# Kernel optimization log

Measured on AMD Instinct MI355X. Metric: run time of the kernel, lower is better.

Reference implementation:

```python
import jax, jax.numpy as jnp
import numpy as np

C = 768
HEADS = 12
NF = 8      # num_frames
SL = 196    # seq_len (patches per frame)
B = 2
N = 1 + NF * SL
HID = 4 * C


def _ln(x, g, b, eps=1e-5):
    mu = jnp.mean(x, axis=-1, keepdims=True)
    var = jnp.mean((x - mu) ** 2, axis=-1, keepdims=True)
    return (x - mu) * jax.lax.rsqrt(var + eps) * g + b


def setup_inputs() -> dict:
    key = jax.random.key(0)
    ks = jax.random.split(key, 16)
    s = 0.02
    return {
        "x": jax.random.normal(ks[0], (B, N, C), jnp.float32),
        "g1": jnp.ones((C,), jnp.float32),
        "b1": jnp.zeros((C,), jnp.float32),
        "Wqkv": jax.random.normal(ks[1], (C, 3 * C), jnp.float32) * s,
        "Wq": jax.random.normal(ks[2], (C, C), jnp.float32) * s,
        "Wkv": jax.random.normal(ks[3], (C, 2 * C), jnp.float32) * s,
        "Wp": jax.random.normal(ks[4], (C, C), jnp.float32) * s,
        "bp": jnp.zeros((C,), jnp.float32),
        "g2": jnp.ones((C,), jnp.float32),
        "b2": jnp.zeros((C,), jnp.float32),
        "W1": jax.random.normal(ks[5], (C, HID), jnp.float32) * s,
        "bf1": jnp.zeros((HID,), jnp.float32),
        "W2": jax.random.normal(ks[6], (HID, C), jnp.float32) * s,
        "bf2": jnp.zeros((C,), jnp.float32),
        "seq_len": SL,
        "num_frames": NF,
    }


def _traj_attn(xn, Wqkv, Wq, Wkv, Wp, bp, P, F):
    Bb, Nn, Cc = xn.shape
    h = HEADS
    d = Cc // h
    scale = d ** -0.5
    S = F * P  # non-cls tokens

    qkv = xn @ Wqkv                                   # (B,N,3C)
    q, k, v = jnp.split(qkv, 3, axis=-1)

    def heads(t):  # (B,N,C) -> (B*h, N, d)
        return t.reshape(Bb, Nn, h, d).transpose(0, 2, 1, 3).reshape(Bb * h, Nn, d)

    q, k, v = heads(q), heads(k), heads(v)
    cls_q, q_ = q[:, :1], q[:, 1:]
    k_ = k[:, 1:]
    v_ = v[:, 1:]

    # cls token attends to all tokens
    sim = jnp.einsum('bid,bjd->bij', cls_q * scale, k)
    cls_out = jnp.einsum('bij,bjd->bid', jax.nn.softmax(sim, axis=-1), v)
    cls_out = cls_out.reshape(Bb, h, 1, d).transpose(0, 2, 1, 3).reshape(Bb, 1, Cc)

    # stage 1: space-only softmax per frame
    qk = jnp.einsum('bqd,bkd->bqk', q_, k_).reshape(Bb * h, S, F, P)
    space_attn = jax.nn.softmax(scale * qk, axis=-1)          # (Bh,S,F,P)
    v_r = v_.reshape(Bb * h, F, P, d)
    x1 = jnp.einsum('bqfn,bfnd->bqfd', space_attn, v_r)       # (Bh,S,F,d)
    x1 = x1.reshape(Bb, h, S, F, d).transpose(0, 2, 3, 1, 4).reshape(Bb, S, F, Cc)

    # diagonal across (query-frame, key-frame)
    xg = x1.reshape(Bb, F, P, F, Cc)
    diag = jnp.diagonal(xg, axis1=1, axis2=3)                 # (B,P,C,F)
    x_diag = diag.transpose(0, 3, 1, 2).reshape(Bb, S, Cc)    # b (f n) d

    # stage 2: frame-wise attention
    q2 = (x_diag @ Wq).reshape(Bb, S, h, d).transpose(0, 2, 1, 3) * scale  # bhsd
    kv2 = x1 @ Wkv
    k2, v2 = jnp.split(kv2, 2, axis=-1)
    k2 = k2.reshape(Bb, S, F, h, d).transpose(0, 3, 1, 2, 4)  # bhsfd
    attn2 = jax.nn.softmax(jnp.einsum('bhsd,bhsfd->bhsf', q2, k2), axis=-1)
    xo = x1.reshape(Bb, S, F, h, d).transpose(0, 3, 1, 2, 4)  # use_original_code=True
    out = jnp.einsum('bhsf,bhsfd->bhsd', attn2, xo)
    out = out.transpose(0, 2, 1, 3).reshape(Bb, S, Cc)

    out = jnp.concatenate([cls_out, out], axis=1) @ Wp + bp
    return out


def reference(x, g1, b1, Wqkv, Wq, Wkv, Wp, bp, g2, b2, W1, bf1, W2, bf2, seq_len, num_frames):
    x = x + _traj_attn(_ln(x, g1, b1), Wqkv, Wq, Wkv, Wp, bp, seq_len, num_frames)
    h = _ln(x, g2, b2)
    h = jax.nn.gelu(h @ W1 + bf1, approximate=False) @ W2 + bf2
    return x + h
```

## Files before the change

### kernel.cpp

```cpp
#include <hip/hip_runtime.h>
#include <hip/hip_bf16.h>
#include <math.h>

#define C     768
#define HEADS 12
#define HD    64
#define NF    8
#define SL    196
#define BB    2
#define NN    1569
#define SS    1568
#define HID   3072
#define CLS_CH 256
#define CLS_NC 7
#define QSCALE 0.18033688011112042f

typedef __attribute__((ext_vector_type(8))) short short8;
typedef __attribute__((ext_vector_type(4))) float f32x4;
typedef unsigned short u16;
typedef unsigned int u32;

__device__ inline float fast_exp2(float x) { return __builtin_amdgcn_exp2f(x); }

__device__ inline u16 f2b(float f) {
    __hip_bfloat16 h = __float2bfloat16(f);
    return *reinterpret_cast<u16*>(&h);
}
__device__ inline float b2f(u16 u) {
    union { unsigned u; float f; } v; v.u = ((unsigned)u) << 16;
    return v.f;
}

__device__ inline void gload_lds16(const void* g, void* l) {
    __builtin_amdgcn_global_load_lds(
        (const __attribute__((address_space(1))) void*)g,
        (__attribute__((address_space(3))) void*)l, 16, 0, 0);
}

__global__ void ln_kernel(const float* __restrict__ x, const float* __restrict__ g,
                          const float* __restrict__ b, u16* __restrict__ out, int rows) {
    int row = blockIdx.x;
    if (row >= rows) return;
    const float* xr = x + (size_t)row * C;
    int tid = threadIdx.x;
    float v[3];
    float sum = 0.f, sumsq = 0.f;
#pragma unroll
    for (int i = 0; i < 3; i++) {
        v[i] = xr[tid + 256 * i];
        sum += v[i]; sumsq += v[i] * v[i];
    }
    __shared__ float s1[4], s2[4];
    for (int off = 32; off; off >>= 1) {
        sum   += __shfl_xor(sum, off);
        sumsq += __shfl_xor(sumsq, off);
    }
    int wave = tid >> 6, lane = tid & 63;
    if (lane == 0) { s1[wave] = sum; s2[wave] = sumsq; }
    __syncthreads();
    sum   = s1[0] + s1[1] + s1[2] + s1[3];
    sumsq = s2[0] + s2[1] + s2[2] + s2[3];
    float mu  = sum / C;
    float var = sumsq / C - mu * mu;
    float rstd = rsqrtf(fmaxf(var, 0.f) + 1e-5f);
    u16* outr = out + (size_t)row * C;
#pragma unroll
    for (int i = 0; i < 3; i++) {
        int c = tid + 256 * i;
        outr[c] = f2b((v[i] - mu) * rstd * g[c] + b[c]);
    }
}

__global__ void wtrans_all_kernel(
    const float* __restrict__ Wqkv, const float* __restrict__ Wq,
    const float* __restrict__ Wkv,  const float* __restrict__ Wp,
    const float* __restrict__ W1,   const float* __restrict__ W2,
    u16* Tqkv, u16* Tq, u16* Tkv, u16* Tp, u16* T1, u16* T2) {
    __shared__ float tile[64][65];
    int bid = blockIdx.x;
    const float* W; u16* Wt; int K, ldb, gx;
    if (bid < 432)       { W = Wqkv; Wt = Tqkv; K = 768;  ldb = 2304; gx = 36; }
    else if (bid < 576)  { W = Wq;   Wt = Tq;   K = 768;  ldb = 768;  gx = 12; bid -= 432; }
    else if (bid < 720)  { W = Wkv;  Wt = Tkv;  K = 768;  ldb = 1536; gx = 12; bid -= 576; }
    else if (bid < 864)  { W = Wp;   Wt = Tp;   K = 768;  ldb = 768;  gx = 12; bid -= 720; }
    else if (bid < 1440) { W = W1;   Wt = T1;   K = 768;  ldb = 3072; gx = 48; bid -= 864; }
    else                 { W = W2;   Wt = T2;   K = 3072; ldb = 768;  gx = 12; bid -= 1440; }
    int nb = (bid % gx) * 64, kb = (bid / gx) * 64;
    int tx = threadIdx.x & 63, ty = threadIdx.x >> 6;
#pragma unroll
    for (int i = 0; i < 64; i += 4)
        tile[ty + i][tx] = W[(size_t)(kb + ty + i) * ldb + nb + tx];
    __syncthreads();
#pragma unroll
    for (int i = 0; i < 64; i += 4)
        Wt[(size_t)(nb + ty + i) * K + kb + tx] = f2b(tile[tx][ty + i]);
}

template<int MODE, int BM, int BN>
__global__ __launch_bounds__(256) void gemm_bf16(
    const u16* __restrict__ A, const u16* __restrict__ Bt,
    const float* __restrict__ bias, const float* resid, void* Cout,
    int M, int N, int K, int lda, int ldb, int gx) {
    constexpr int MT   = BM / 32;
    constexpr int NT   = BN / 32;
    constexpr int ACH  = BM * 4;
    constexpr int TCH  = (BM + BN) * 4;
    constexpr int HALF = (BM + BN) * 64;
    __shared__ char smem[2 * HALF];
    int tid = threadIdx.x, lane = tid & 63, wave = tid >> 6;
    int wr = wave >> 1, wc = wave & 1;
    int r16 = lane & 15, kg = lane >> 4;

    int nwg = gridDim.x, orig = blockIdx.x;
    int qq = nwg >> 3, rr = nwg & 7, xcd = orig & 7, lid = orig >> 3;
    int wg = (xcd < rr ? xcd * (qq + 1) : rr * (qq + 1) + (xcd - rr) * qq) + lid;
    int bx = wg % gx, by = wg / gx;
    if constexpr (MODE == 4) {
        int mt_ = (M + BM - 1) / BM;
        int chunk = by / mt_; by -= chunk * mt_;
        A    += (size_t)chunk * K;
        Bt   += (size_t)chunk * K;
        Cout  = (void*)((float*)Cout + (size_t)chunk * ((size_t)M * N));
    }
    int row0 = by * BM, col0 = bx * BN;

    f32x4 acc[MT][NT];
#pragma unroll
    for (int mt = 0; mt < MT; mt++)
#pragma unroll
        for (int nt = 0; nt < NT; nt++) acc[mt][nt] = (f32x4){0.f, 0.f, 0.f, 0.f};

    auto stage = [&](char* dstbase, int ks) {
        int k0 = ks << 5;
#pragma unroll
        for (int it = 0; it < TCH / 256; it++) {
            int c = it * 256 + tid;
            const u16* src;
            if (c < ACH) {
                int ml = c >> 2, s = c & 3;
                int kgs = s ^ ((ml >> 1) & 3);
                int gm = row0 + ml; if (gm >= M) gm = M - 1;
                src = A + (size_t)gm * lda + k0 + kgs * 8;
            } else {
                int cc = c - ACH;
                int nl = cc >> 2, s = cc & 3;
                int kgs = s ^ ((nl >> 1) & 3);
                src = Bt + (size_t)(col0 + nl) * ldb + k0 + kgs * 8;
            }
            gload_lds16(src, dstbase + it * 4096 + wave * 1024);
        }
    };

    int nsteps = K >> 5;
    stage(smem, 0);
    __syncthreads();
    for (int ks = 0; ks < nsteps; ks++) {
        char* curb = smem + (ks & 1) * HALF;
        if (ks + 1 < nsteps) stage(smem + ((ks + 1) & 1) * HALF, ks + 1);
        short8 af[MT], bfr[NT];
#pragma unroll
        for (int mt = 0; mt < MT; mt++) {
            int ml = wr * (BM / 2) + mt * 16 + r16;
            af[mt] = *(const short8*)(curb + ml * 64 + ((kg ^ ((ml >> 1) & 3)) << 4));
        }
#pragma unroll
        for (int nt = 0; nt < NT; nt++) {
            int nl = wc * (BN / 2) + nt * 16 + r16;
            bfr[nt] = *(const short8*)(curb + BM * 64 + nl * 64 + ((kg ^ ((nl >> 1) & 3)) << 4));
        }
        __builtin_amdgcn_s_setprio(1);
#pragma unroll
        for (int mt = 0; mt < MT; mt++)
#pragma unroll
            for (int nt = 0; nt < NT; nt++)
                acc[mt][nt] = __builtin_amdgcn_mfma_f32_16x16x32_bf16(af[mt], bfr[nt], acc[mt][nt], 0, 0, 0);
        __builtin_amdgcn_s_setprio(0);
        __syncthreads();
    }
#pragma unroll
    for (int mt = 0; mt < MT; mt++) {
#pragma unroll
        for (int r2 = 0; r2 < 4; r2++) {
            int gm = row0 + wr * (BM / 2) + mt * 16 + kg * 4 + r2;
            if (gm >= M) continue;
#pragma unroll
            for (int nt = 0; nt < NT; nt++) {
                int gn = col0 + wc * (BN / 2) + nt * 16 + r16;
                float v = acc[mt][nt][r2];
                if constexpr (MODE == 1) {
                    v += bias[gn];
                    v = 0.5f * v * (1.f + erff(v * 0.70710678118f));
                }
                if constexpr (MODE == 2) {
                    v += bias[gn] + resid[(size_t)gm * N + gn];
                    ((float*)Cout)[(size_t)gm * N + gn] = v;
                } else if constexpr (MODE == 4) {
                    ((float*)Cout)[(size_t)gm * N + gn] = v;
                } else {
                    if constexpr (MODE == 3) { if (gn < 768) v *= QSCALE; }
                    ((u16*)Cout)[(size_t)gm * N + gn] = f2b(v);
                }
            }
        }
    }
}

__global__ void fc2_merge_kernel(const float* __restrict__ p,
                                 const float* __restrict__ bias, float* __restrict__ out) {
    int i = blockIdx.x * 256 + threadIdx.x;
    int total = BB * NN * (C / 4);
    if (i >= total) return;
    int c4 = i % (C / 4);
    size_t stride = (size_t)BB * NN * (C / 4);
    float4 bb = ((const float4*)bias)[c4];
    float4 a0 = ((const float4*)p)[i];
    float4 a1 = ((const float4*)p)[i + stride];
    float4 o  = ((float4*)out)[i];
    o.x += a0.x + a1.x + bb.x;
    o.y += a0.y + a1.y + bb.y;
    o.z += a0.z + a1.z + bb.z;
    o.w += a0.w + a1.w + bb.w;
    ((float4*)out)[i] = o;
}

__global__ void cls_partial_kernel(const u16* __restrict__ qkv, float* __restrict__ part) {
    int c = blockIdx.x, bh = blockIdx.y;
    int b = bh / HEADS, hh = bh % HEADS;
    int tid = threadIdx.x;
    int wave = tid >> 6, lane = tid & 63;
    __shared__ float s_q[HD];
    __shared__ float s_sc[CLS_CH];
    __shared__ float sm[4], ss[4];
    __shared__ float sacc[4][HD];
    if (tid < HD) s_q[tid] = b2f(qkv[(size_t)(b * NN) * 2304 + hh * HD + tid]);
    __syncthreads();

    int j0 = c * CLS_CH;
    int j = j0 + tid;
    float sc = -1e30f;
    if (j < NN) {
        const short8* kp = (const short8*)(qkv + ((size_t)(b * NN) + j) * 2304 + C + hh * HD);
        float acc = 0.f;
#pragma unroll
        for (int u = 0; u < 8; u++) {
            short8 kv = kp[u];
#pragma unroll
            for (int e = 0; e < 8; e++) acc += s_q[u * 8 + e] * b2f((u16)kv[e]);
        }
        sc = acc;
    }
    float m = sc;
    for (int off = 32; off; off >>= 1) m = fmaxf(m, __shfl_xor(m, off));
    if (lane == 0) sm[wave] = m;
    __syncthreads();
    m = fmaxf(fmaxf(sm[0], sm[1]), fmaxf(sm[2], sm[3]));
    float e = (j < NN) ? fast_exp2(sc - m) : 0.f;
    s_sc[tid] = e;
    float su = e;
    for (int off = 32; off; off >>= 1) su += __shfl_xor(su, off);
    if (lane == 0) ss[wave] = su;
    __syncthreads();
    float ssum = ss[0] + ss[1] + ss[2] + ss[3];

    int jj = tid >> 6, d = tid & 63;
    int jmax = NN - j0; if (jmax > CLS_CH) jmax = CLS_CH;
    const u16* vcol = qkv + ((size_t)(b * NN) + j0) * 2304 + 2 * C + hh * HD + d;
    float acc = 0.f;
    for (int t = jj; t < jmax; t += 4)
        acc += s_sc[t] * b2f(vcol[(size_t)t * 2304]);
    sacc[jj][d] = acc;
    __syncthreads();
    if (tid < HD) {
        float pv = sacc[0][tid] + sacc[1][tid] + sacc[2][tid] + sacc[3][tid];
        float* pp = part + ((size_t)bh * CLS_NC + c) * 66;
        pp[2 + tid] = pv;
        if (tid == 0) { pp[0] = m; pp[1] = ssum; }
    }
}

__global__ void cls_reduce_kernel(const float* __restrict__ part, u16* __restrict__ y) {
    int bh = blockIdx.x;
    int b = bh / HEADS, hh = bh % HEADS;
    int d = threadIdx.x;
    float gm = -1e30f;
#pragma unroll
    for (int c = 0; c < CLS_NC; c++)
        gm = fmaxf(gm, part[((size_t)bh * CLS_NC + c) * 66]);
    float tot = 0.f, pv = 0.f;
#pragma unroll
    for (int c = 0; c < CLS_NC; c++) {
        const float* pp = part + ((size_t)bh * CLS_NC + c) * 66;
        float w = fast_exp2(pp[0] - gm);
        tot += pp[1] * w;
        pv  += pp[2 + d] * w;
    }
    y[(size_t)(b * NN) * C + hh * HD + d] = f2b(pv / tot);
}

__global__ void repack_kv_kernel(const u16* __restrict__ qkv,
                                 u16* __restrict__ Kb, u16* __restrict__ Vt) {
    const int NK = 24 * NF * 208 * 8;
    const int NV = 24 * NF * 64 * 28;
    int t = blockIdx.x * 256 + threadIdx.x;
    if (t < NK) {
        int d8 = t & 7;
        int rest = t >> 3;
        int n = rest % 208;
        rest /= 208;
        int f = rest % NF;
        int bh = rest / NF;
        int b = bh / HEADS, h = bh % HEADS;
        short8 v = {0, 0, 0, 0, 0, 0, 0, 0};
        if (n < SL)
            v = *(const short8*)(qkv + ((size_t)(b * NN) + 1 + f * SL + n) * 2304 + C + h * HD + d8 * 8);
        *(short8*)(Kb + (((size_t)bh * NF + f) * 208 + n) * 64 + d8 * 8) = v;
    } else {
        int u = t - NK;
        if (u >= NV) return;
        int n8 = u % 28;
        int rest = u / 28;
        int d = rest % 64;
        rest /= 64;
        int f = rest % NF;
        int bh = rest / NF;
        int b = bh / HEADS, h = bh % HEADS;
        int n0 = n8 * 8;
        const u16* src = qkv + ((size_t)(b * NN) + 1 + f * SL) * 2304 + 2 * C + h * HD + d;
        short8 v;
#pragma unroll
        for (int jj = 0; jj < 8; jj++) {
            int n = n0 + jj;
            v[jj] = (n < SL) ? (short)src[(size_t)n * 2304] : (short)0;
        }
        *(short8*)(Vt + (((size_t)bh * NF + f) * 64 + d) * 224 + n0) = v;
    }
}

__global__ void space_attn_mfma(
    const u16* __restrict__ qkv, const u16* __restrict__ Kb,
    const u16* __restrict__ Vt, u16* __restrict__ x1, u16* __restrict__ xd) {
    __shared__ u16 smem[14848];
    int tid = threadIdx.x;
    int lane = tid & 63, wave = tid >> 6;
    int r16 = lane & 15, kg = lane >> 4;

    int n = blockIdx.x;
    int xcd = n & 7;
    int slot = n >> 3;
    int j = slot % 25;
    int gw = slot / 25;
    int bh = xcd * 3 + gw % 3;
    int f = gw / 3;
    int b = bh / HEADS, h = bh % HEADS;

    int strip = j * 4 + wave;
    bool act = strip < 98;
    if (!act) strip = 97;
    int q0 = strip * 16;

    const u16* qrow = qkv + ((size_t)(b * NN) + 1 + q0 + r16) * 2304 + h * HD + kg * 8;
    short8 aq0 = *(const short8*)(qrow);
    short8 aq1 = *(const short8*)(qrow + 32);

    const char* kb_g = (const char*)(Kb + ((size_t)bh * NF + f) * 208 * 64);
    for (int w = wave; w < 26; w += 4) {
        int p = w * 1024 + lane * 16;
        int row = p >> 7;
        int src = (p & ~127) | ((p & 127) ^ ((row & 7) << 4));
        gload_lds16(kb_g + src, (char*)smem + p);
    }
    __syncthreads();

    f32x4 acc[13];
#pragma unroll
    for (int t = 0; t < 13; t++) acc[t] = (f32x4){0.f, 0.f, 0.f, 0.f};
    const char* ksm = (const char*)smem;
    int swz = (r16 & 7) << 4;
    __builtin_amdgcn_s_setprio(1);
#pragma unroll
    for (int t = 0; t < 13; t++) {
        const char* krow = ksm + (t * 16 + r16) * 128;
        short8 bk0 = *(const short8*)(krow + ((kg * 16) ^ swz));
        short8 bk1 = *(const short8*)(krow + ((64 + kg * 16) ^ swz));
        acc[t] = __builtin_amdgcn_mfma_f32_16x16x32_bf16(bk0, aq0, acc[t], 0, 0, 0);
        acc[t] = __builtin_amdgcn_mfma_f32_16x16x32_bf16(bk1, aq1, acc[t], 0, 0, 0);
    }
    __builtin_amdgcn_s_setprio(0);

    const u16* vbase = Vt + ((size_t)bh * NF + f) * 64 * 224;
    short8 vf[2][4];
#pragma unroll
    for (int dt = 0; dt < 4; dt++)
        vf[0][dt] = *(const short8*)(vbase + (dt * 16 + r16) * 224 + kg * 8);

    __syncthreads();
    u16* pb = smem + wave * 3712;

    bool tailz = (kg >= 1);
    float ssum = 0.f;
    float pv_[13][4];
#pragma unroll
    for (int t = 0; t < 13; t++) {
#pragma unroll
        for (int r = 0; r < 4; r++) {
            float p = (t == 12 && tailz) ? 0.f : fast_exp2(acc[t][r]);
            pv_[t][r] = p;
            ssum += p;
        }
    }
    ssum += __shfl_xor(ssum, 16);
    ssum += __shfl_xor(ssum, 32);
    float inv = 1.f / ssum;

#pragma unroll
    for (int t = 0; t < 13; t++) {
        u32 w0 = (u32)f2b(pv_[t][0] * inv) | ((u32)f2b(pv_[t][1] * inv) << 16);
        u32 w1 = (u32)f2b(pv_[t][2] * inv) | ((u32)f2b(pv_[t][3] * inv) << 16);
        *(uint2*)(&pb[r16 * 232 + t * 16 + kg * 4]) = (uint2){w0, w1};
    }
    {
        int zr = lane >> 2, zc = 208 + (lane & 3) * 4;
        *(uint2*)(&pb[zr * 232 + zc]) = (uint2){0u, 0u};
    }

    f32x4 o[4];
#pragma unroll
    for (int dt = 0; dt < 4; dt++) o[dt] = (f32x4){0.f, 0.f, 0.f, 0.f};
    __builtin_amdgcn_s_setprio(1);
#pragma unroll
    for (int kc = 0; kc < 7; kc++) {
        if (kc < 6) {
#pragma unroll
            for (int dt = 0; dt < 4; dt++)
                vf[(kc + 1) & 1][dt] = *(const short8*)(vbase + (dt * 16 + r16) * 224 + (kc + 1) * 32 + kg * 8);
        }
        short8 pa = *(const short8*)(&pb[r16 * 232 + kc * 32 + kg * 8]);
#pragma unroll
        for (int dt = 0; dt < 4; dt++)
            o[dt] = __builtin_amdgcn_mfma_f32_16x16x32_bf16(pa, vf[kc & 1][dt], o[dt], 0, 0, 0);
    }
    __builtin_amdgcn_s_setprio(0);

    if (act) {
#pragma unroll
        for (int dt = 0; dt < 4; dt++)
#pragma unroll
            for (int r = 0; r < 4; r++)
                pb[(kg * 4 + r) * 72 + dt * 16 + r16] = f2b(o[dt][r]);
        u16* x1row = x1 + (((size_t)(b * SS + q0)) * NF + f) * C + h * HD;
        u16* xdrow = xd + ((size_t)(b * SS + q0)) * C + h * HD;
        int fbase = f * SL;
#pragma unroll
        for (int it = 0; it < 2; it++) {
            int c = it * 64 + lane;
            int qr = c >> 3, c8 = c & 7;
            short8 v8 = *(const short8*)(&pb[qr * 72 + c8 * 8]);
            *(short8*)(x1row + (size_t)qr * (NF * C) + c8 * 8) = v8;
            if ((unsigned)(q0 + qr - fbase) < (unsigned)SL)
                *(short8*)(xdrow + (size_t)qr * C + c8 * 8) = v8;
        }
    }
}

__global__ void attn2_kernel(const u16* __restrict__ q2, const u16* __restrict__ k2,
                             const u16* __restrict__ x1, u16* __restrict__ y) {
    int item = blockIdx.x * 4 + (threadIdx.x >> 6);
    if (item >= BB * HEADS * SS) return;
    int lane = threadIdx.x & 63;
    int s = item % SS;
    int bh = item / SS;
    int b = bh / HEADS, hh = bh % HEADS;
    size_t rowbs = (size_t)(b * SS + s);
    float qv = b2f(q2[rowbs * C + hh * HD + lane]) * QSCALE;
    float lg[NF];
#pragma unroll
    for (int f = 0; f < NF; f++) {
        float p = qv * b2f(k2[(rowbs * NF + f) * C + hh * HD + lane]);
        for (int off = 32; off; off >>= 1) p += __shfl_xor(p, off);
        lg[f] = p;
    }
    float m = lg[0];
#pragma unroll
    for (int f = 1; f < NF; f++) m = fmaxf(m, lg[f]);
    float sum = 0.f;
#pragma unroll
    for (int f = 0; f < NF; f++) { lg[f] = fast_exp2(lg[f] - m); sum += lg[f]; }
    float inv = 1.f / sum;
    float acc = 0.f;
#pragma unroll
    for (int f = 0; f < NF; f++) acc += lg[f] * b2f(x1[(rowbs * NF + f) * C + hh * HD + lane]);
    y[((size_t)(b * NN) + 1 + s) * C + hh * HD + lane] = f2b(acc * inv);
}

extern "C" void kernel_launch(void* const* d_in, const int* in_sizes, int n_in,
                              void* d_out, int out_size, void* d_ws, size_t ws_size,
                              hipStream_t stream) {
    const float* x    = (const float*)d_in[0];
    const float* g1   = (const float*)d_in[1];
    const float* b1   = (const float*)d_in[2];
    const float* Wqkv = (const float*)d_in[3];
    const float* Wq   = (const float*)d_in[4];
    const float* Wkv  = (const float*)d_in[5];
    const float* Wp   = (const float*)d_in[6];
    const float* bp   = (const float*)d_in[7];
    const float* g2   = (const float*)d_in[8];
    const float* b2_  = (const float*)d_in[9];
    const float* W1   = (const float*)d_in[10];
    const float* bf1  = (const float*)d_in[11];
    const float* W2   = (const float*)d_in[12];
    const float* bf2  = (const float*)d_in[13];
    float* out = (float*)d_out;

    u16* us     = (u16*)d_ws;
    u16* xn_b   = us;
    u16* qkv_b  = xn_b   + 2409984;
    u16* Wt_qkv = qkv_b  + 7229952;
    u16* Wt_q   = Wt_qkv + 1769472;
    u16* Wt_kv  = Wt_q   + 589824;
    u16* Wt_p   = Wt_kv  + 589824;
    u16* W1t    = Wt_p   + 589824;
    u16* W2t    = W1t    + 2359296;
    u16* Kb     = W2t    + 2359296;
    u16* Vt     = Kb     + 2555904;
    u16* x1b    = Vt     + 2752512;
    u16* xdb    = x1b    + 19267584;
    u16* q2b    = xdb    + 2408448;
    u16* k2b    = q2b    + 2408448;
    u16* y_b    = k2b    + 19267584;
    u16* a1b    = y_b    + 2409984;
    float* cls_ws   = (float*)(a1b + 9639936);
    float* fc2_part = cls_ws + 24 * 7 * 66;

    const int M1 = BB * NN;
    const int M2 = BB * SS;
    const int M3 = BB * SS * NF;

    wtrans_all_kernel<<<2016, 256, 0, stream>>>(Wqkv, Wq, Wkv, Wp, W1, W2,
                                                Wt_qkv, Wt_q, Wt_kv, Wt_p, W1t, W2t);
    ln_kernel<<<M1, 256, 0, stream>>>(x, g1, b1, xn_b, M1);
    gemm_bf16<3, 128, 64><<<36 * 25, 256, 0, stream>>>(
        xn_b, Wt_qkv, nullptr, nullptr, qkv_b, M1, 2304, 768, 768, 768, 36);
    repack_kv_kernel<<<(24 * NF * 208 * 8 + 24 * NF * 64 * 28 + 255) / 256, 256, 0, stream>>>(
        qkv_b, Kb, Vt);
    cls_partial_kernel<<<dim3(CLS_NC, BB * HEADS), 256, 0, stream>>>(qkv_b, cls_ws);
    cls_reduce_kernel<<<BB * HEADS, 64, 0, stream>>>(cls_ws, y_b);
    space_attn_mfma<<<4800, 256, 0, stream>>>(qkv_b, Kb, Vt, x1b, xdb);
    gemm_bf16<0, 64, 64><<<12 * 49, 256, 0, stream>>>(
        xdb, Wt_q, nullptr, nullptr, q2b, M2, 768, 768, 768, 768, 12);
    gemm_bf16<0, 128, 128><<<6 * 196, 256, 0, stream>>>(
        x1b, Wt_kv, nullptr, nullptr, k2b, M3, 768, 768, 768, 768, 6);
    attn2_kernel<<<(BB * HEADS * SS + 3) / 4, 256, 0, stream>>>(q2b, k2b, x1b, y_b);
    gemm_bf16<2, 64, 64><<<12 * 50, 256, 0, stream>>>(
        y_b, Wt_p, bp, x, out, M1, 768, 768, 768, 768, 12);
    ln_kernel<<<M1, 256, 0, stream>>>(out, g2, b2_, xn_b, M1);
    gemm_bf16<1, 128, 64><<<48 * 25, 256, 0, stream>>>(
        xn_b, W1t, bf1, nullptr, a1b, M1, 3072, 768, 768, 768, 48);
    gemm_bf16<4, 128, 64><<<12 * 25 * 2, 256, 0, stream>>>(
        a1b, W2t, nullptr, nullptr, fc2_part, M1, 768, 1536, 3072, 3072, 12);
    fc2_merge_kernel<<<(BB * NN * (C / 4) + 255) / 256, 256, 0, stream>>>(
        fc2_part, bf2, out);
}
```

Baseline: 291.8 us.

## Reassociate stage-2 logits to avoid the full K2 projection over all frames

Instead of projecting every x1 token through Wkv to build k2 (a large GEMM with M = B*S*F), the per-head query is folded into the key weights: u = q2_h · Wk_h^T is computed per head with a small GEMM. The logits are then taken as dot products of u with raw x1 rows inside a new fused attention kernel that stages u and x1 in LDS. This removes the big 12544x768x768 GEMM and the k2 buffer. In exchange it adds a 12-head-batched GEMM, a larger u buffer, and a 768-long dot product per head per frame in the attention kernel.

```diff
diff --git a/kernel.cpp b/kernel.cpp
--- a/kernel.cpp
+++ b/kernel.cpp
@@ -78,15 +78,21 @@
     u16* Tqkv, u16* Tq, u16* Tkv, u16* Tp, u16* T1, u16* T2) {
     __shared__ float tile[64][65];
     int bid = blockIdx.x;
-    const float* W; u16* Wt; int K, ldb, gx;
+    const float* W; u16* Wt; int K, ldb, gx; bool notr = false;
     if (bid < 432)       { W = Wqkv; Wt = Tqkv; K = 768;  ldb = 2304; gx = 36; }
     else if (bid < 576)  { W = Wq;   Wt = Tq;   K = 768;  ldb = 768;  gx = 12; bid -= 432; }
-    else if (bid < 720)  { W = Wkv;  Wt = Tkv;  K = 768;  ldb = 1536; gx = 12; bid -= 576; }
+    else if (bid < 720)  { W = Wkv;  Wt = Tkv;  K = 768;  ldb = 1536; gx = 12; bid -= 576; notr = true; }
     else if (bid < 864)  { W = Wp;   Wt = Tp;   K = 768;  ldb = 768;  gx = 12; bid -= 720; }
     else if (bid < 1440) { W = W1;   Wt = T1;   K = 768;  ldb = 3072; gx = 48; bid -= 864; }
     else                 { W = W2;   Wt = T2;   K = 3072; ldb = 768;  gx = 12; bid -= 1440; }
     int nb = (bid % gx) * 64, kb = (bid / gx) * 64;
     int tx = threadIdx.x & 63, ty = threadIdx.x >> 6;
+    if (notr) {
+#pragma unroll
+        for (int i = 0; i < 64; i += 4)
+            Wt[(size_t)(kb + ty + i) * 768 + nb + tx] = f2b(W[(size_t)(kb + ty + i) * ldb + nb + tx]);
+        return;
+    }
 #pragma unroll
     for (int i = 0; i < 64; i += 4)
         tile[ty + i][tx] = W[(size_t)(kb + ty + i) * ldb + nb + tx];
@@ -114,7 +120,14 @@
     int nwg = gridDim.x, orig = blockIdx.x;
     int qq = nwg >> 3, rr = nwg & 7, xcd = orig & 7, lid = orig >> 3;
     int wg = (xcd < rr ? xcd * (qq + 1) : rr * (qq + 1) + (xcd - rr) * qq) + lid;
-    int bx = wg % gx, by = wg / gx;
+    int bx, by, h5 = 0;
+    if constexpr (MODE == 5) {
+        bx = wg % 12; int tmp = wg / 12; by = tmp % 49; h5 = tmp / 49;
+        A  += h5 * 64;
+        Bt += h5 * 64;
+    } else {
+        bx = wg % gx; by = wg / gx;
+    }
     if constexpr (MODE == 4) {
         int mt_ = (M + BM - 1) / BM;
         int chunk = by / mt_; by -= chunk * mt_;
@@ -196,6 +209,8 @@
                     ((float*)Cout)[(size_t)gm * N + gn] = v;
                 } else if constexpr (MODE == 4) {
                     ((float*)Cout)[(size_t)gm * N + gn] = v;
+                } else if constexpr (MODE == 5) {
+                    ((u16*)Cout)[((size_t)gm * 12 + h5) * 768 + gn] = f2b(v * QSCALE);
                 } else {
                     if constexpr (MODE == 3) { if (gn < 768) v *= QSCALE; }
                     ((u16*)Cout)[(size_t)gm * N + gn] = f2b(v);
@@ -462,34 +477,59 @@
     }
 }
 
-__global__ void attn2_kernel(const u16* __restrict__ q2, const u16* __restrict__ k2,
-                             const u16* __restrict__ x1, u16* __restrict__ y) {
-    int item = blockIdx.x * 4 + (threadIdx.x >> 6);
-    if (item >= BB * HEADS * SS) return;
-    int lane = threadIdx.x & 63;
-    int s = item % SS;
-    int bh = item / SS;
-    int b = bh / HEADS, hh = bh % HEADS;
-    size_t rowbs = (size_t)(b * SS + s);
-    float qv = b2f(q2[rowbs * C + hh * HD + lane]) * QSCALE;
-    float lg[NF];
-#pragma unroll
-    for (int f = 0; f < NF; f++) {
-        float p = qv * b2f(k2[(rowbs * NF + f) * C + hh * HD + lane]);
-        for (int off = 32; off; off >>= 1) p += __shfl_xor(p, off);
-        lg[f] = p;
-    }
-    float m = lg[0];
-#pragma unroll
-    for (int f = 1; f < NF; f++) m = fmaxf(m, lg[f]);
-    float sum = 0.f;
-#pragma unroll
-    for (int f = 0; f < NF; f++) { lg[f] = fast_exp2(lg[f] - m); sum += lg[f]; }
-    float inv = 1.f / sum;
-    float acc = 0.f;
-#pragma unroll
-    for (int f = 0; f < NF; f++) acc += lg[f] * b2f(x1[(rowbs * NF + f) * C + hh * HD + lane]);
-    y[((size_t)(b * NN) + 1 + s) * C + hh * HD + lane] = f2b(acc * inv);
+__global__ __launch_bounds__(256) void attn2_fused(
+    const u16* __restrict__ u, const u16* __restrict__ x1, u16* __restrict__ y) {
+    __shared__ u16 smem[15360];
+    int tid = threadIdx.x;
+    int lane = tid & 63, wave = tid >> 6;
+    int sidx = blockIdx.x;
+    int b = sidx / SS, s = sidx % SS;
+
+    const u16* ubase = u  + (size_t)sidx * 12 * 768;
+    const u16* xbase = x1 + (size_t)sidx * NF * 768;
+#pragma unroll
+    for (int it = 0; it < 8; it++) {
+        int c = it * 256 + tid;
+        if (c < 1920) {
+            const u16* src = (c < 1152) ? (ubase + c * 8) : (xbase + (c - 1152) * 8);
+            gload_lds16(src, (char*)smem + c * 16);
+        }
+    }
+    __syncthreads();
+    const u16* su = smem;
+    const u16* sx = smem + 9216;
+
+#pragma unroll
+    for (int hh = 0; hh < 3; hh++) {
+        int h = wave * 3 + hh;
+        float sc[NF];
+#pragma unroll
+        for (int f = 0; f < NF; f++) sc[f] = 0.f;
+#pragma unroll
+        for (int cc = 0; cc < 12; cc++) {
+            int c = cc * 64 + lane;
+            float uv = b2f(su[h * 768 + c]);
+#pragma unroll
+            for (int f = 0; f < NF; f++)
+                sc[f] += b2f(sx[f * 768 + c]) * uv;
+        }
+#pragma unroll
+        for (int off = 32; off; off >>= 1)
+#pragma unroll
+            for (int f = 0; f < NF; f++) sc[f] += __shfl_xor(sc[f], off);
+        float m = sc[0];
+#pragma unroll
+        for (int f = 1; f < NF; f++) m = fmaxf(m, sc[f]);
+        float sum = 0.f;
+#pragma unroll
+        for (int f = 0; f < NF; f++) { sc[f] = fast_exp2(sc[f] - m); sum += sc[f]; }
+        float inv = 1.f / sum;
+        float acc = 0.f;
+#pragma unroll
+        for (int f = 0; f < NF; f++)
+            acc += sc[f] * b2f(sx[f * 768 + h * 64 + lane]);
+        y[((size_t)b * NN + 1 + s) * C + h * 64 + lane] = f2b(acc * inv);
+    }
 }
 
 extern "C" void kernel_launch(void* const* d_in, const int* in_sizes, int n_in,
@@ -516,8 +556,8 @@
     u16* qkv_b  = xn_b   + 2409984;
     u16* Wt_qkv = qkv_b  + 7229952;
     u16* Wt_q   = Wt_qkv + 1769472;
-    u16* Wt_kv  = Wt_q   + 589824;
-    u16* Wt_p   = Wt_kv  + 589824;
+    u16* Wkv_b  = Wt_q   + 589824;
+    u16* Wt_p   = Wkv_b  + 589824;
     u16* W1t    = Wt_p   + 589824;
     u16* W2t    = W1t    + 2359296;
     u16* Kb     = W2t    + 2359296;
@@ -525,18 +565,17 @@
     u16* x1b    = Vt     + 2752512;
     u16* xdb    = x1b    + 19267584;
     u16* q2b    = xdb    + 2408448;
-    u16* k2b    = q2b    + 2408448;
-    u16* y_b    = k2b    + 19267584;
+    u16* u_b    = q2b    + 2408448;
+    u16* y_b    = u_b    + 28901376;
     u16* a1b    = y_b    + 2409984;
     float* cls_ws   = (float*)(a1b + 9639936);
     float* fc2_part = cls_ws + 24 * 7 * 66;
 
     const int M1 = BB * NN;
     const int M2 = BB * SS;
-    const int M3 = BB * SS * NF;
 
     wtrans_all_kernel<<<2016, 256, 0, stream>>>(Wqkv, Wq, Wkv, Wp, W1, W2,
-                                                Wt_qkv, Wt_q, Wt_kv, Wt_p, W1t, W2t);
+                                                Wt_qkv, Wt_q, Wkv_b, Wt_p, W1t, W2t);
     ln_kernel<<<M1, 256, 0, stream>>>(x, g1, b1, xn_b, M1);
     gemm_bf16<3, 128, 64><<<36 * 25, 256, 0, stream>>>(
         xn_b, Wt_qkv, nullptr, nullptr, qkv_b, M1, 2304, 768, 768, 768, 36);
@@ -547,9 +586,9 @@
     space_attn_mfma<<<4800, 256, 0, stream>>>(qkv_b, Kb, Vt, x1b, xdb);
     gemm_bf16<0, 64, 64><<<12 * 49, 256, 0, stream>>>(
         xdb, Wt_q, nullptr, nullptr, q2b, M2, 768, 768, 768, 768, 12);
-    gemm_bf16<0, 128, 128><<<6 * 196, 256, 0, stream>>>(
-        x1b, Wt_kv, nullptr, nullptr, k2b, M3, 768, 768, 768, 768, 6);
-    attn2_kernel<<<(BB * HEADS * SS + 3) / 4, 256, 0, stream>>>(q2b, k2b, x1b, y_b);
+    gemm_bf16<5, 64, 64><<<7056, 256, 0, stream>>>(
+        q2b, Wkv_b, nullptr, nullptr, u_b, M2, 768, 64, 768, 768, 12);
+    attn2_fused<<<M2, 256, 0, stream>>>(u_b, x1b, y_b);
     gemm_bf16<2, 64, 64><<<12 * 50, 256, 0, stream>>>(
         y_b, Wt_p, bp, x, out, M1, 768, 768, 768, 768, 12);
     ln_kernel<<<M1, 256, 0, stream>>>(out, g2, b2_, xn_b, M1);
```

Measured after the change: 302.9 us. +3.8%, slower.
